# Optimization experiments

Hardware: AMD Instinct MI355X
Metric: run time of the kernel (lower is better)

Reference implementation:

```python
import jax, jax.numpy as jnp
import numpy as np

K = 3
PAD = 1
STRIDE = 1
DIL = 1


def _conv(x, w, b):
    # standard 3x3 conv, NCHW / OIHW
    y = jax.lax.conv_general_dilated(
        x, w, (STRIDE, STRIDE), [(PAD, PAD), (PAD, PAD)],
        rhs_dilation=(DIL, DIL),
        dimension_numbers=('NCHW', 'OIHW', 'NCHW'))
    return y + b[None, :, None, None]


def _deform_conv2d(x, offset, mask, weight, bias):
    # x: [B,C,H,W]; offset: [B,2*KK,Ho,Wo] (y,x interleaved per kernel tap);
    # mask: [B,KK,Ho,Wo]; weight: [Co,C,K,K]; bias: [Co]
    B, C, H, W = x.shape
    KK = K * K
    Ho, Wo = offset.shape[2], offset.shape[3]

    off = offset.reshape(B, KK, 2, Ho, Wo)
    dy, dx = off[:, :, 0], off[:, :, 1]          # [B,KK,Ho,Wo]

    ky, kx = jnp.meshgrid(jnp.arange(K), jnp.arange(K), indexing='ij')
    ky = ky.reshape(KK).astype(x.dtype)
    kx = kx.reshape(KK).astype(x.dtype)
    hs = (jnp.arange(Ho) * STRIDE - PAD).astype(x.dtype)
    ws = (jnp.arange(Wo) * STRIDE - PAD).astype(x.dtype)
    base_y = hs[None, :, None] + (ky * DIL)[:, None, None]   # [KK,Ho,1]
    base_x = ws[None, None, :] + (kx * DIL)[:, None, None]   # [KK,1,Wo]

    py = base_y[None] + dy                        # [B,KK,Ho,Wo] sample rows
    px = base_x[None] + dx                        # sample cols

    y0 = jnp.floor(py)
    x0 = jnp.floor(px)
    ly = py - y0                                  # bilinear fractional weights
    lx = px - x0
    y0i = y0.astype(jnp.int32)
    x0i = x0.astype(jnp.int32)

    flat = x.reshape(B, C, H * W)

    def gather(iy, ix):
        # zero-padded gather at integer locations -> [B,C,KK,Ho,Wo]
        valid = (iy >= 0) & (iy < H) & (ix >= 0) & (ix < W)
        iyc = jnp.clip(iy, 0, H - 1)
        ixc = jnp.clip(ix, 0, W - 1)
        idx = (iyc * W + ixc).reshape(B, 1, KK * Ho * Wo)
        g = jnp.take_along_axis(flat, jnp.broadcast_to(idx, (B, C, KK * Ho * Wo)), axis=2)
        g = g.reshape(B, C, KK, Ho, Wo)
        return g * valid[:, None].astype(x.dtype)

    val = (gather(y0i, x0i) * ((1 - ly) * (1 - lx))[:, None]
           + gather(y0i, x0i + 1) * ((1 - ly) * lx)[:, None]
           + gather(y0i + 1, x0i) * (ly * (1 - lx))[:, None]
           + gather(y0i + 1, x0i + 1) * (ly * lx)[:, None])

    val = val * mask[:, None]                     # DCNv2 modulation

    wr = weight.reshape(weight.shape[0], C, KK)   # [Co,C,KK]
    out = jnp.einsum('bckhw,ock->bohw', val, wr)
    return out + bias[None, :, None, None]


def setup_inputs() -> dict:
    key = jax.random.key(0)
    ks = jax.random.split(key, 7)
    B, C, Co, H, W = 4, 128, 256, 96, 96
    KK = K * K
    x = jax.random.normal(ks[0], (B, C, H, W), dtype=jnp.float32)
    weight = jax.random.normal(ks[1], (Co, C, K, K), dtype=jnp.float32) * 0.03
    bias = jax.random.normal(ks[2], (Co,), dtype=jnp.float32) * 0.01
    offset_w = jax.random.normal(ks[3], (2 * KK, C, K, K), dtype=jnp.float32) * 0.01
    offset_b = jax.random.normal(ks[4], (2 * KK,), dtype=jnp.float32) * 0.01
    mod_w = jax.random.normal(ks[5], (KK, C, K, K), dtype=jnp.float32) * 0.01
    mod_b = jnp.ones((KK,), dtype=jnp.float32)
    return {'x': x, 'weight': weight, 'bias': bias,
            'offset_w': offset_w, 'offset_b': offset_b,
            'mod_w': mod_w, 'mod_b': mod_b}


def reference(x, weight, bias, offset_w, offset_b, mod_w, mod_b):
    offset = _conv(x, offset_w, offset_b)
    mask = jax.nn.sigmoid(_conv(x, mod_w, mod_b))
    return _deform_conv2d(x, offset, mask, weight, bias)
```

## Files before the change

kernel.cpp:

```cpp
#include <hip/hip_runtime.h>
#include <math.h>

#define HH 96
#define WW 96
#define HW 9216
#define CIN 128
#define COUT 256

typedef _Float16 f16;
typedef _Float16 f16x2 __attribute__((ext_vector_type(2)));
typedef _Float16 f16x8 __attribute__((ext_vector_type(8)));
typedef __attribute__((ext_vector_type(4))) float f32x4;

static __device__ __forceinline__ unsigned short f2h(float f) {
  union { f16 h; unsigned short u; } v; v.h = (f16)f; return v.u;
}

__global__ __launch_bounds__(256) void k_prep(const float* __restrict__ x,
                                              const float* __restrict__ offw,
                                              const float* __restrict__ modw,
                                              const float* __restrict__ wgt,
                                              unsigned short* __restrict__ xTh,
                                              unsigned short* __restrict__ wAbF,
                                              unsigned short* __restrict__ wTtF) {
  __shared__ float tile[32][129];
  int bid = blockIdx.x;
  int t = threadIdx.x;
  if (bid < 1152) {
    int wseg = bid % 3, h = (bid / 3) % 96, b = bid / 288;
    int wl = t & 31, cg = t >> 5;
    const float* xp = x + ((size_t)(b * 128 + cg) * 96 + h) * 96 + wseg * 32 + wl;
#pragma unroll
    for (int i = 0; i < 16; ++i)
      tile[wl][cg + 8 * i] = xp[(size_t)8 * i * HW];
    __syncthreads();
    int cl = t & 127, wg = t >> 7;
    unsigned short* op = xTh + (((size_t)(b * 96 + h) * 96) + wseg * 32) * 128 + cl;
#pragma unroll
    for (int i = 0; i < 16; ++i)
      op[(size_t)(wg + 2 * i) * 128] = f2h(tile[wg + 2 * i][cl]);
  } else if (bid < 1296) {
    int i = (bid - 1152) * 256 + t;
    if (i < 9 * 2 * 4 * 512) {
      int j = i & 7;
      int l = (i >> 3) & 63;
      int ks = (i >> 9) & 3;
      int ng = i >> 11;
      int kpos = ng >> 1, n16 = ng & 1;
      int n = n16 * 16 + (l & 15);
      int c = ks * 32 + (l >> 4) * 8 + j;
      float v = 0.f;
      if (n < 18) v = offw[n * 1152 + c * 9 + kpos];
      else if (n < 27) v = modw[(n - 18) * 1152 + c * 9 + kpos];
      wAbF[i] = f2h(v);
    }
  } else {
    int i = (bid - 1296) * 256 + t;
    if (i < 9 * 16 * 4 * 512) {
      int j = i & 7;
      int l = (i >> 3) & 63;
      int ks = (i >> 9) & 3;
      int ng = i >> 11;
      int kpos = ng >> 4, n16 = ng & 15;
      int n = n16 * 16 + (l & 15);
      int c = ks * 32 + (l >> 4) * 8 + j;
      wTtF[i] = f2h(wgt[n * 1152 + c * 9 + kpos]);
    }
  }
}

__global__ __launch_bounds__(256) void k_main(const unsigned short* __restrict__ xTh,
                                              const unsigned short* __restrict__ wAbF,
                                              const unsigned short* __restrict__ wTtF,
                                              const float* __restrict__ offb,
                                              const float* __restrict__ modb,
                                              const float* __restrict__ bias,
                                              float* __restrict__ out) {
  __shared__ __align__(16) unsigned short Ab[32 * 136];
  __shared__ float om_lds[27 * 33];
  __shared__ float ez[4 * 1040];

  int t = threadIdx.x;
  int l = t & 63, w = t >> 6;
  int lm = l & 15, lq = l >> 4;
  int raw = blockIdx.x;
  int bid = (raw & 7) * 144 + (raw >> 3);
  int pix0 = bid * 32;
  int b = pix0 / HW;
  int posim0 = pix0 % HW;
  int ibase = b * HW;

  {
    int mh = w & 1, n16o = w >> 1;
    int prow = pix0 + mh * 16 + lm;
    int pimo = prow % HW;
    int hoo = pimo / 96, woo = pimo % 96;
    f32x4 acco = (f32x4){0.f, 0.f, 0.f, 0.f};
    const f16x8 zv = {0, 0, 0, 0, 0, 0, 0, 0};
#pragma unroll 1
    for (int kpos = 0; kpos < 9; ++kpos) {
      int dyr = kpos / 3 - 1, dxr = kpos % 3 - 1;
      bool valid = ((unsigned)(hoo + dyr) < 96u) && ((unsigned)(woo + dxr) < 96u);
      int srow = valid ? (prow + dyr * 96 + dxr) : prow;
      const unsigned short* ap = xTh + (size_t)srow * 128 + lq * 8;
      const unsigned short* bp = wAbF + (size_t)((kpos * 2 + n16o) * 4) * 512 + l * 8;
#pragma unroll
      for (int ks = 0; ks < 4; ++ks) {
        f16x8 af = valid ? *(const f16x8*)(ap + ks * 32) : zv;
        f16x8 bf = *(const f16x8*)(bp + (size_t)ks * 512);
        acco = __builtin_amdgcn_mfma_f32_16x16x32_f16(af, bf, acco, 0, 0, 0);
      }
    }
    int n = n16o * 16 + lm;
    if (n < 27) {
      float bv = (n < 18) ? offb[n] : modb[n - 18];
#pragma unroll
      for (int r = 0; r < 4; ++r) {
        float v = acco[r] + bv;
        if (n >= 18) v = 1.f / (1.f + expf(-v));
        om_lds[n * 33 + mh * 16 + lq * 4 + r] = v;
      }
    }
  }
  __syncthreads();

  int pxo = t >> 3;
  int sc8 = t & 7;
  int pimS = (pix0 + pxo) % HW;
  int hoS = pimS / 96, woS = pimS % 96;

  f32x4 acc[2][4];
#pragma unroll
  for (int i = 0; i < 2; ++i)
#pragma unroll
    for (int j = 0; j < 4; ++j)
      acc[i][j] = (f32x4){0.f, 0.f, 0.f, 0.f};

  for (int kpos = 0; kpos < 9; ++kpos) {
    float dy = om_lds[(2 * kpos) * 33 + pxo];
    float dx = om_lds[(2 * kpos + 1) * 33 + pxo];
    float mk = om_lds[(18 + kpos) * 33 + pxo];
    float py = (float)(hoS - 1 + kpos / 3) + dy;
    float pxf = (float)(woS - 1 + kpos % 3) + dx;
    float fy = floorf(py), fx = floorf(pxf);
    int y0 = (int)fy, x0 = (int)fx;
    float ly = py - fy, lx = pxf - fx;
    float w00 = (1.f - ly) * (1.f - lx), w01 = (1.f - ly) * lx;
    float w10 = ly * (1.f - lx),         w11 = ly * lx;
    bool vy0 = (unsigned)y0 < 96u, vy1 = (unsigned)(y0 + 1) < 96u;
    bool vx0 = (unsigned)x0 < 96u, vx1 = (unsigned)(x0 + 1) < 96u;
    w00 = (vy0 && vx0) ? w00 * mk : 0.f;
    w01 = (vy0 && vx1) ? w01 * mk : 0.f;
    w10 = (vy1 && vx0) ? w10 * mk : 0.f;
    w11 = (vy1 && vx1) ? w11 * mk : 0.f;
    int y0c = min(max(y0, 0), 95), y1c = min(max(y0 + 1, 0), 95);
    int x0c = min(max(x0, 0), 95), x1c = min(max(x0 + 1, 0), 95);
    int ofs[4];
    ofs[0] = (ibase + y0c * 96 + x0c) * 128;
    ofs[1] = (ibase + y0c * 96 + x1c) * 128;
    ofs[2] = (ibase + y1c * 96 + x0c) * 128;
    ofs[3] = (ibase + y1c * 96 + x1c) * 128;
    f16 h00 = (f16)w00, h01 = (f16)w01, h10 = (f16)w10, h11 = (f16)w11;
    f16x2 wp[4];
    wp[0] = (f16x2){h00, h00}; wp[1] = (f16x2){h01, h01};
    wp[2] = (f16x2){h10, h10}; wp[3] = (f16x2){h11, h11};

    uint4 q[4][2];
#pragma unroll
    for (int c = 0; c < 4; ++c)
#pragma unroll
      for (int it = 0; it < 2; ++it)
        q[c][it] = *(const uint4*)(xTh + ofs[c] + (sc8 + 8 * it) * 8);

    __syncthreads();
#pragma unroll
    for (int it = 0; it < 2; ++it) {
      union { uint4 u; f16x2 h[4]; } a0, a1, a2, a3;
      a0.u = q[0][it]; a1.u = q[1][it]; a2.u = q[2][it]; a3.u = q[3][it];
      union { f16x8 v; f16x2 h[4]; } r;
#pragma unroll
      for (int j = 0; j < 4; ++j)
        r.h[j] = a0.h[j] * wp[0] + a1.h[j] * wp[1] + a2.h[j] * wp[2] + a3.h[j] * wp[3];
      *(f16x8*)(Ab + pxo * 136 + (sc8 + 8 * it) * 8) = r.v;
    }
    __syncthreads();

#pragma unroll
    for (int ks = 0; ks < 4; ++ks) {
      f16x8 af[2], bfv[4];
#pragma unroll
      for (int mt = 0; mt < 2; ++mt)
        af[mt] = *(const f16x8*)(Ab + (mt * 16 + lm) * 136 + ks * 32 + lq * 8);
      const unsigned short* bp =
          wTtF + (size_t)((kpos * 16 + w * 4) * 4 + ks) * 512 + l * 8;
#pragma unroll
      for (int nt = 0; nt < 4; ++nt)
        bfv[nt] = *(const f16x8*)(bp + (size_t)nt * 4 * 512);
#pragma unroll
      for (int mt = 0; mt < 2; ++mt)
#pragma unroll
        for (int nt = 0; nt < 4; ++nt)
          acc[mt][nt] = __builtin_amdgcn_mfma_f32_16x16x32_f16(af[mt], bfv[nt], acc[mt][nt], 0, 0, 0);
    }
  }

  float bias_v[4];
#pragma unroll
  for (int nt = 0; nt < 4; ++nt) bias_v[nt] = bias[w * 64 + nt * 16 + lm];
  float* z = ez + w * 1040;
#pragma unroll
  for (int mt = 0; mt < 2; ++mt) {
    __syncthreads();
#pragma unroll
    for (int nt = 0; nt < 4; ++nt)
#pragma unroll
      for (int r = 0; r < 4; ++r)
        z[(lq * 4 + r) * 65 + nt * 16 + lm] = acc[mt][nt][r] + bias_v[nt];
    __syncthreads();
    int pxr = l & 15;
    int nb = l >> 4;
#pragma unroll
    for (int s = 0; s < 16; ++s) {
      int n = nb + 4 * s;
      out[((size_t)(b * COUT + w * 64 + n)) * HW + posim0 + mt * 16 + pxr] = z[pxr * 65 + n];
    }
  }
}

extern "C" void kernel_launch(void* const* d_in, const int* in_sizes, int n_in,
                              void* d_out, int out_size, void* d_ws, size_t ws_size,
                              hipStream_t stream) {
  const float* x      = (const float*)d_in[0];
  const float* weight = (const float*)d_in[1];
  const float* bias   = (const float*)d_in[2];
  const float* offw   = (const float*)d_in[3];
  const float* offb   = (const float*)d_in[4];
  const float* modw   = (const float*)d_in[5];
  const float* modb   = (const float*)d_in[6];
  float* out = (float*)d_out;
  float* ws = (float*)d_ws;

  unsigned short* xTh  = (unsigned short*)ws;
  unsigned short* wTtF = (unsigned short*)(ws + 2359296);
  unsigned short* wAbF = (unsigned short*)(ws + 2359296 + 147456);

  k_prep<<<2448, 256, 0, stream>>>(x, offw, modw, weight, xTh, wAbF, wTtF);
  k_main<<<1152, 256, 0, stream>>>(xTh, wAbF, wTtF, offb, modb, bias, out);
}
```

Measured before the change: 149.6 us.

## Double-buffer the deformable-sampled tile to overlap gathers with MFMA

```diff
diff --git a/kernel.cpp b/kernel.cpp
--- a/kernel.cpp
+++ b/kernel.cpp
@@ -69,14 +69,14 @@
   }
 }
 
-__global__ __launch_bounds__(256) void k_main(const unsigned short* __restrict__ xTh,
-                                              const unsigned short* __restrict__ wAbF,
-                                              const unsigned short* __restrict__ wTtF,
-                                              const float* __restrict__ offb,
-                                              const float* __restrict__ modb,
-                                              const float* __restrict__ bias,
-                                              float* __restrict__ out) {
-  __shared__ __align__(16) unsigned short Ab[32 * 136];
+__global__ __launch_bounds__(256, 4) void k_main(const unsigned short* __restrict__ xTh,
+                                                 const unsigned short* __restrict__ wAbF,
+                                                 const unsigned short* __restrict__ wTtF,
+                                                 const float* __restrict__ offb,
+                                                 const float* __restrict__ modb,
+                                                 const float* __restrict__ bias,
+                                                 float* __restrict__ out) {
+  __shared__ __align__(16) unsigned short Ab[2][32 * 136];
   __shared__ float om_lds[27 * 33];
   __shared__ float ez[4 * 1040];
 
@@ -136,12 +136,15 @@
     for (int j = 0; j < 4; ++j)
       acc[i][j] = (f32x4){0.f, 0.f, 0.f, 0.f};
 
-  for (int kpos = 0; kpos < 9; ++kpos) {
-    float dy = om_lds[(2 * kpos) * 33 + pxo];
-    float dx = om_lds[(2 * kpos + 1) * 33 + pxo];
-    float mk = om_lds[(18 + kpos) * 33 + pxo];
-    float py = (float)(hoS - 1 + kpos / 3) + dy;
-    float pxf = (float)(woS - 1 + kpos % 3) + dx;
+  f16x2 wp[4];
+  uint4 q[4][2];
+
+  {
+    float dy = om_lds[0 * 33 + pxo];
+    float dx = om_lds[1 * 33 + pxo];
+    float mk = om_lds[18 * 33 + pxo];
+    float py = (float)(hoS - 1) + dy;
+    float pxf = (float)(woS - 1) + dx;
     float fy = floorf(py), fx = floorf(pxf);
     int y0 = (int)fy, x0 = (int)fx;
     float ly = py - fy, lx = pxf - fx;
@@ -161,18 +164,13 @@
     ofs[2] = (ibase + y1c * 96 + x0c) * 128;
     ofs[3] = (ibase + y1c * 96 + x1c) * 128;
     f16 h00 = (f16)w00, h01 = (f16)w01, h10 = (f16)w10, h11 = (f16)w11;
-    f16x2 wp[4];
     wp[0] = (f16x2){h00, h00}; wp[1] = (f16x2){h01, h01};
     wp[2] = (f16x2){h10, h10}; wp[3] = (f16x2){h11, h11};
-
-    uint4 q[4][2];
 #pragma unroll
     for (int c = 0; c < 4; ++c)
 #pragma unroll
       for (int it = 0; it < 2; ++it)
         q[c][it] = *(const uint4*)(xTh + ofs[c] + (sc8 + 8 * it) * 8);
-
-    __syncthreads();
 #pragma unroll
     for (int it = 0; it < 2; ++it) {
       union { uint4 u; f16x2 h[4]; } a0, a1, a2, a3;
@@ -181,16 +179,57 @@
 #pragma unroll
       for (int j = 0; j < 4; ++j)
         r.h[j] = a0.h[j] * wp[0] + a1.h[j] * wp[1] + a2.h[j] * wp[2] + a3.h[j] * wp[3];
-      *(f16x8*)(Ab + pxo * 136 + (sc8 + 8 * it) * 8) = r.v;
-    }
-    __syncthreads();
+      *(f16x8*)(&Ab[0][0] + pxo * 136 + (sc8 + 8 * it) * 8) = r.v;
+    }
+  }
+  __syncthreads();
+
+#pragma unroll 1
+  for (int kpos = 0; kpos < 9; ++kpos) {
+    unsigned short* buf = &Ab[kpos & 1][0];
+    unsigned short* nbuf = &Ab[(kpos & 1) ^ 1][0];
+
+    if (kpos < 8) {
+      int kp = kpos + 1;
+      float dy = om_lds[(2 * kp) * 33 + pxo];
+      float dx = om_lds[(2 * kp + 1) * 33 + pxo];
+      float mk = om_lds[(18 + kp) * 33 + pxo];
+      float py = (float)(hoS - 1 + kp / 3) + dy;
+      float pxf = (float)(woS - 1 + kp % 3) + dx;
+      float fy = floorf(py), fx = floorf(pxf);
+      int y0 = (int)fy, x0 = (int)fx;
+      float ly = py - fy, lx = pxf - fx;
+      float w00 = (1.f - ly) * (1.f - lx), w01 = (1.f - ly) * lx;
+      float w10 = ly * (1.f - lx),         w11 = ly * lx;
+      bool vy0 = (unsigned)y0 < 96u, vy1 = (unsigned)(y0 + 1) < 96u;
+      bool vx0 = (unsigned)x0 < 96u, vx1 = (unsigned)(x0 + 1) < 96u;
+      w00 = (vy0 && vx0) ? w00 * mk : 0.f;
+      w01 = (vy0 && vx1) ? w01 * mk : 0.f;
+      w10 = (vy1 && vx0) ? w10 * mk : 0.f;
+      w11 = (vy1 && vx1) ? w11 * mk : 0.f;
+      int y0c = min(max(y0, 0), 95), y1c = min(max(y0 + 1, 0), 95);
+      int x0c = min(max(x0, 0), 95), x1c = min(max(x0 + 1, 0), 95);
+      int ofs[4];
+      ofs[0] = (ibase + y0c * 96 + x0c) * 128;
+      ofs[1] = (ibase + y0c * 96 + x1c) * 128;
+      ofs[2] = (ibase + y1c * 96 + x0c) * 128;
+      ofs[3] = (ibase + y1c * 96 + x1c) * 128;
+      f16 h00 = (f16)w00, h01 = (f16)w01, h10 = (f16)w10, h11 = (f16)w11;
+      wp[0] = (f16x2){h00, h00}; wp[1] = (f16x2){h01, h01};
+      wp[2] = (f16x2){h10, h10}; wp[3] = (f16x2){h11, h11};
+#pragma unroll
+      for (int c = 0; c < 4; ++c)
+#pragma unroll
+        for (int it = 0; it < 2; ++it)
+          q[c][it] = *(const uint4*)(xTh + ofs[c] + (sc8 + 8 * it) * 8);
+    }
 
 #pragma unroll
     for (int ks = 0; ks < 4; ++ks) {
       f16x8 af[2], bfv[4];
 #pragma unroll
       for (int mt = 0; mt < 2; ++mt)
-        af[mt] = *(const f16x8*)(Ab + (mt * 16 + lm) * 136 + ks * 32 + lq * 8);
+        af[mt] = *(const f16x8*)(buf + (mt * 16 + lm) * 136 + ks * 32 + lq * 8);
       const unsigned short* bp =
           wTtF + (size_t)((kpos * 16 + w * 4) * 4 + ks) * 512 + l * 8;
 #pragma unroll
@@ -202,6 +241,20 @@
         for (int nt = 0; nt < 4; ++nt)
           acc[mt][nt] = __builtin_amdgcn_mfma_f32_16x16x32_f16(af[mt], bfv[nt], acc[mt][nt], 0, 0, 0);
     }
+
+    if (kpos < 8) {
+#pragma unroll
+      for (int it = 0; it < 2; ++it) {
+        union { uint4 u; f16x2 h[4]; } a0, a1, a2, a3;
+        a0.u = q[0][it]; a1.u = q[1][it]; a2.u = q[2][it]; a3.u = q[3][it];
+        union { f16x8 v; f16x2 h[4]; } r;
+#pragma unroll
+        for (int j = 0; j < 4; ++j)
+          r.h[j] = a0.h[j] * wp[0] + a1.h[j] * wp[1] + a2.h[j] * wp[2] + a3.h[j] * wp[3];
+        *(f16x8*)(nbuf + pxo * 136 + (sc8 + 8 * it) * 8) = r.v;
+      }
+    }
+    __syncthreads();
   }
 
   float bias_v[4];
@@ -210,13 +263,11 @@
   float* z = ez + w * 1040;
 #pragma unroll
   for (int mt = 0; mt < 2; ++mt) {
-    __syncthreads();
 #pragma unroll
     for (int nt = 0; nt < 4; ++nt)
 #pragma unroll
       for (int r = 0; r < 4; ++r)
         z[(lq * 4 + r) * 65 + nt * 16 + lm] = acc[mt][nt][r] + bias_v[nt];
-    __syncthreads();
     int pxr = l & 15;
     int nb = l >> 4;
 #pragma unroll
```

Measured after the change: 172.2 us. 1.15x slower.
